# Optimization experiments

Hardware: AMD Instinct MI355X
Metric: run time of the kernel (lower is better)

Reference implementation:

```python
import jax, jax.numpy as jnp
import numpy as np

B, H, NQ, NK, D = 2, 16, 4096, 4096, 64


def _attn_with_lse(q, k, v, scale):
    # q: [B,H,p,d], k: [B,H,s,d], v: [B,H,s,dv]
    s = jnp.einsum('bhqd,bhkd->bhqk', q, k) * scale
    lse = jax.nn.logsumexp(s, axis=-1, keepdims=True)  # [B,H,p,1]
    p = jnp.exp(s - lse)
    o = jnp.einsum('bhqk,bhkd->bhqd', p, v)
    return o, lse


def setup_inputs() -> dict:
    key = jax.random.key(0)
    k1, k2, k3 = jax.random.split(key, 3)
    return {
        'query': jax.random.normal(k1, (B, H, NQ, D), dtype=jnp.float32),
        'key': jax.random.normal(k2, (B, H, NK, D), dtype=jnp.float32),
        'value': jax.random.normal(k3, (B, H, NK, D), dtype=jnp.float32),
        'n_query_groups': 4,
        'n_key_groups': 4,
    }


def reference(query, key, value, n_query_groups, n_key_groups):
    b, h, nq, d = query.shape
    nk = key.shape[2]
    m, n = int(n_query_groups), int(n_key_groups)
    scale = d ** (-0.5)
    pq, pk = nq // m, nk // n  # group sizes n_gp
    c0, c1 = m // 2, n // 2   # center groups c_gp

    # representative query/key blocks
    q_gp = query[:, :, c0 * pq:(c0 + 1) * pq, :]              # [B,H,pq,d]
    k_gp = key[:, :, c1 * pk:(c1 + 1) * pk, :]                # [B,H,pk,d]
    # value chunks concatenated on feature dim (zero-padding of q/k in the
    # original leaves the dot products unchanged, so we skip it)
    v_gp = value.reshape(b, h, n, pk, d).transpose(0, 1, 3, 2, 4).reshape(b, h, pk, n * d)
    attn_gp, lse_gp = _attn_with_lse(q_gp, k_gp, v_gp, scale)  # [B,H,pq,n*d], [B,H,pq,1]

    # sample one key per key group (torch uses random.randint; fixed to 0 here)
    k_picked = 0
    k_sample = key[:, :, k_picked::pk, :]                      # [B,H,n,d]
    w = jnp.einsum('bhqd,bhnd->bhqn', query, k_sample)         # [B,H,nq,n]
    w_gps = w.reshape(b, h, m, pq, n)
    norm_gps = jnp.linalg.norm(w_gps, axis=-2)                 # [B,H,m,n]
    s_gps = norm_gps / norm_gps[:, :, c0, c1][:, :, None, None]

    v_sum = value.reshape(b, h, n, pk, d).sum(axis=3)          # [B,H,n,d]
    om = jnp.maximum(1.0 - s_gps, 0.0)                         # clamp(1-s, min=0)
    num_part1 = om[:, :, :, :, None, None] * v_sum[:, :, None, :, None, :]  # [B,H,m,n,1,d]
    den_part1 = (om * pk)[:, :, :, :, None, None]              # [B,H,m,n,1,1]

    lse_exp = jnp.exp(lse_gp)                                  # [B,H,pq,1]
    unnorm = lse_exp * attn_gp                                 # [B,H,pq,n*d]
    attn_gps = unnorm.reshape(b, h, pq, n, d).transpose(0, 1, 3, 2, 4)  # [B,H,n,pq,d]
    num_part2 = s_gps[:, :, :, :, None, None] * attn_gps[:, :, None, :, :, :]  # [B,H,m,n,pq,d]
    den_part2 = s_gps[:, :, :, :, None, None] * lse_exp[:, :, None, None, :, :]  # [B,H,m,n,pq,1]

    num_agg = (num_part1 + num_part2).sum(axis=3)              # [B,H,m,pq,d]
    den_agg = (den_part1 + den_part2).sum(axis=3)              # [B,H,m,pq,1]

    attn = (num_agg / den_agg).reshape(b, h, nq, d)
    lse = jnp.log(den_agg).reshape(b, h, nq, 1)
    return attn, lse
```

## Files before the change

kernel.cpp:

```cpp
#include <hip/hip_runtime.h>
#include <hip/hip_bf16.h>


#define BH_TOT 32
#define SEQ    4096
#define DIM    64
#define PQ     1024

#define QB_OFF 34816u
#define KB_OFF (QB_OFF + 4u*1024u*1024u)
#define VB_OFF (KB_OFF + 4u*1024u*1024u)
#define WS_NEED (VB_OFF + 16u*1024u*1024u)

#define QSCALE 0.1803368801111204f

typedef __attribute__((ext_vector_type(8))) short bf16x8;
typedef __attribute__((ext_vector_type(4))) short bf16x4;
typedef __attribute__((ext_vector_type(4))) float f32x4;
typedef __attribute__((ext_vector_type(4))) _Float16 f16x4;
typedef __attribute__((ext_vector_type(8))) _Float16 f16x8;

__device__ __forceinline__ short f2bf(float x) {
    unsigned u = __float_as_uint(x);
    u = u + 0x7fffu + ((u >> 16) & 1u);
    return (short)(u >> 16);
}
__device__ __forceinline__ float bf2f(unsigned short h) {
    return __uint_as_float(((unsigned)h) << 16);
}

__global__ __launch_bounds__(256) void prep_norm2(
    const float* __restrict__ query, const float* __restrict__ key,
    float* __restrict__ ws)
{
    __shared__ float ksm[4][64];
    __shared__ float wsum[4][16];
    const int t = threadIdx.x;
    const int bh = blockIdx.x >> 2, gi = blockIdx.x & 3;
    if (t < 64) ws[512 + blockIdx.x * 64 + t] = 0.f;
    ksm[t >> 6][t & 63] = key[((size_t)bh * SEQ + (size_t)(t >> 6) * PQ) * DIM + (t & 63)];
    __syncthreads();
    const int wv = t >> 6, lane = t & 63, c = lane & 15, hi = lane >> 4;
    bf16x8 bb0, bb1;
#pragma unroll
    for (int j = 0; j < 8; ++j) {
        bb0[j] = (c < 4) ? f2bf(ksm[c][hi * 8 + j]) : (short)0;
        bb1[j] = (c < 4) ? f2bf(ksm[c][32 + hi * 8 + j]) : (short)0;
    }
    float acc0 = 0.f, acc1 = 0.f, acc2 = 0.f, acc3 = 0.f;
    const float* qbase = query + ((size_t)bh * SEQ + (size_t)gi * PQ) * DIM;
    for (int it = 0; it < 16; ++it) {
        const int row = (wv * 16 + it) * 16 + c;
        const float* qp = qbase + (size_t)row * 64 + hi * 8;
        float4 a0 = *(const float4*)qp;
        float4 a1 = *(const float4*)(qp + 4);
        float4 a2 = *(const float4*)(qp + 32);
        float4 a3 = *(const float4*)(qp + 36);
        bf16x8 qa0, qa1;
        qa0[0] = f2bf(a0.x); qa0[1] = f2bf(a0.y); qa0[2] = f2bf(a0.z); qa0[3] = f2bf(a0.w);
        qa0[4] = f2bf(a1.x); qa0[5] = f2bf(a1.y); qa0[6] = f2bf(a1.z); qa0[7] = f2bf(a1.w);
        qa1[0] = f2bf(a2.x); qa1[1] = f2bf(a2.y); qa1[2] = f2bf(a2.z); qa1[3] = f2bf(a2.w);
        qa1[4] = f2bf(a3.x); qa1[5] = f2bf(a3.y); qa1[6] = f2bf(a3.z); qa1[7] = f2bf(a3.w);
        f32x4 s = (f32x4){0.f, 0.f, 0.f, 0.f};
        s = __builtin_amdgcn_mfma_f32_16x16x32_bf16(qa0, bb0, s, 0, 0, 0);
        s = __builtin_amdgcn_mfma_f32_16x16x32_bf16(qa1, bb1, s, 0, 0, 0);
        acc0 += s[0] * s[0]; acc1 += s[1] * s[1];
        acc2 += s[2] * s[2]; acc3 += s[3] * s[3];
    }
    float asum = acc0 + acc1 + acc2 + acc3;
    asum += __shfl_xor(asum, 16);
    asum += __shfl_xor(asum, 32);
    if (lane < 16) wsum[wv][lane] = asum;
    __syncthreads();
    if (t < 4) ws[bh * 16 + gi * 4 + t] = wsum[0][t] + wsum[1][t] + wsum[2][t] + wsum[3][t];
}

__global__ __launch_bounds__(256) void conv_qk(
    const float* __restrict__ query, const float* __restrict__ key,
    char* __restrict__ wsb)
{
    const int t = threadIdx.x;
    if (blockIdx.x < 512) {
        const int bh = blockIdx.x >> 4, qt = blockIdx.x & 15;
#pragma unroll
        for (int i = 0; i < 2; ++i) {
            const int sid = t + i * 256;
            const int mt = sid >> 7, kh = (sid >> 6) & 1, lane = sid & 63;
            const int c = lane & 15, hi = lane >> 4;
            const float* p = query + ((size_t)bh * SEQ + 2048 + qt * 64 + mt * 16 + c) * DIM
                             + kh * 32 + hi * 8;
            float4 a = *(const float4*)p, b = *(const float4*)(p + 4);
            bf16x8 h;
            h[0] = f2bf(a.x * QSCALE); h[1] = f2bf(a.y * QSCALE);
            h[2] = f2bf(a.z * QSCALE); h[3] = f2bf(a.w * QSCALE);
            h[4] = f2bf(b.x * QSCALE); h[5] = f2bf(b.y * QSCALE);
            h[6] = f2bf(b.z * QSCALE); h[7] = f2bf(b.w * QSCALE);
            const size_t fidx = ((size_t)(bh * 16 + qt) * 4 + mt) * 2 + kh;
            *(bf16x8*)(wsb + QB_OFF + fidx * 1024 + lane * 16) = h;
        }
    } else {
        const int b2 = blockIdx.x - 512;
        const int bh = b2 >> 4, kc = b2 & 15;
#pragma unroll
        for (int i = 0; i < 2; ++i) {
            const int sid = t + i * 256;
            const int kh = sid >> 8, nt = (sid >> 6) & 3, lane = sid & 63;
            const int c = lane & 15, hi = lane >> 4;
            const float* p = key + ((size_t)bh * SEQ + 2048 + kc * 64 + nt * 16 + c) * DIM
                             + kh * 32 + hi * 8;
            float4 a = *(const float4*)p, b = *(const float4*)(p + 4);
            bf16x8 h;
            h[0] = f2bf(a.x); h[1] = f2bf(a.y); h[2] = f2bf(a.z); h[3] = f2bf(a.w);
            h[4] = f2bf(b.x); h[5] = f2bf(b.y); h[6] = f2bf(b.z); h[7] = f2bf(b.w);
            const size_t fidx = ((size_t)(bh * 16 + kc) * 2 + kh) * 4 + nt;
            *(bf16x8*)(wsb + KB_OFF + fidx * 1024 + lane * 16) = h;
        }
    }
}

__global__ __launch_bounds__(256) void conv_v(
    const float* __restrict__ value, char* __restrict__ wsb, float* __restrict__ ws)
{
    __shared__ float Ls[64][68];
    __shared__ float ps[4][64];
    const int t = threadIdx.x;
    const int blk = blockIdx.x;
    const int bh = blk >> 6, gj = (blk >> 4) & 3, kc = blk & 15;
    const float* src = value + ((size_t)bh * SEQ + gj * PQ + kc * 64) * DIM;
#pragma unroll
    for (int i = 0; i < 4; ++i) {
        const int u = t + i * 256;
        const int row = u >> 4, c4 = (u & 15) * 4;
        *(float4*)&Ls[row][c4] = *(const float4*)(src + row * 64 + c4);
    }
    __syncthreads();
    {
        const int d = t & 63, rg = t >> 6;
        float s = 0.f;
#pragma unroll
        for (int i = 0; i < 16; ++i) s += Ls[rg * 16 + i][d];
        ps[rg][d] = s;
    }
    __syncthreads();
    if (t < 64) {
        float tot = ps[0][t] + ps[1][t] + ps[2][t] + ps[3][t];
        atomicAdd(&ws[512 + bh * 256 + gj * 64 + t], tot);
    }
#pragma unroll
    for (int i = 0; i < 2; ++i) {
        const int sid = t + i * 256;
        const int pl = sid >> 8, dt = (sid >> 6) & 3, lane = sid & 63;
        const int c = lane & 15, hi = lane >> 4;
        f16x8 h;
#pragma unroll
        for (int j = 0; j < 8; ++j)
            h[j] = (_Float16)Ls[pl * 32 + hi * 8 + j][dt * 16 + c];
        const size_t off = ((((size_t)(bh * 4 + gj) * 32 + kc * 2 + pl) * 4 + dt) * 64 + lane) * 16;
        *(f16x8*)(wsb + VB_OFF + off) = h;
    }
}

__global__ __launch_bounds__(256, 4) void kattn4(
    const char* __restrict__ wsb, float* __restrict__ out)
{
    __shared__ union {
        _Float16 Pf[2][2][2][512];
        float Uf[32][257];
    } lds;
    __shared__ float Llds[32];

    const int blk = blockIdx.x;
    const int slot = blk >> 3;
    const int bh = (blk & 7) * 4 + (slot >> 5);
    const int qt = slot & 31;
    const int t = threadIdx.x;
    const int w = t >> 6, lane = t & 63;
    const int c = lane & 15, hi = lane >> 4;

    bf16x8 aq[2][2];
#pragma unroll
    for (int qt2 = 0; qt2 < 2; ++qt2) {
        const int s = qt * 2 + qt2;
        const size_t fr = ((size_t)(bh * 16 + (s >> 2)) * 4 + (s & 3)) * 2;
        aq[qt2][0] = *(const bf16x8*)(wsb + QB_OFF + fr * 1024 + lane * 16);
        aq[qt2][1] = *(const bf16x8*)(wsb + QB_OFF + (fr + 1) * 1024 + lane * 16);
    }
    const char* kb = wsb + KB_OFF + ((size_t)(bh * 16) * 8) * 1024 + (size_t)w * 1024 + lane * 16;
    const char* vb = wsb + VB_OFF + ((size_t)(bh * 4 + w) * 128) * 1024 + lane * 16;

    f32x4 Uacc[2][4];
#pragma unroll
    for (int mt = 0; mt < 2; ++mt)
#pragma unroll
        for (int dt = 0; dt < 4; ++dt)
            Uacc[mt][dt] = (f32x4){0.f, 0.f, 0.f, 0.f};
    f32x4 Lacc[2];
    Lacc[0] = (f32x4){0.f, 0.f, 0.f, 0.f};
    Lacc[1] = (f32x4){0.f, 0.f, 0.f, 0.f};
    f16x8 kOnes;
#pragma unroll
    for (int j = 0; j < 8; ++j) kOnes[j] = (_Float16)1.f;

    const int k0 = w * 16 + hi * 4;
    const int pspan = k0 >> 5;
    const int pidx = (c + 16 * ((k0 & 31) >> 3)) * 8 + (k0 & 7);

    bf16x8 bk0 = *(const bf16x8*)(kb);
    bf16x8 bk1 = *(const bf16x8*)(kb + 4096);

    for (int kc = 0; kc < 16; ++kc) {
        const int buf = kc & 1;
        const char* vcb = vb + (size_t)kc * 8192;
        f16x8 vf[8];
#pragma unroll
        for (int u = 0; u < 8; ++u) vf[u] = *(const f16x8*)(vcb + u * 1024);
        f32x4 sacc[2];
        __builtin_amdgcn_s_setprio(1);
#pragma unroll
        for (int qt2 = 0; qt2 < 2; ++qt2) {
            f32x4 s = (f32x4){0.f, 0.f, 0.f, 0.f};
            s = __builtin_amdgcn_mfma_f32_16x16x32_bf16(bk0, aq[qt2][0], s, 0, 0, 0);
            s = __builtin_amdgcn_mfma_f32_16x16x32_bf16(bk1, aq[qt2][1], s, 0, 0, 0);
            sacc[qt2] = s;
        }
        __builtin_amdgcn_s_setprio(0);
        if (kc < 15) {
            bk0 = *(const bf16x8*)(kb + (size_t)(kc + 1) * 8192);
            bk1 = *(const bf16x8*)(kb + (size_t)(kc + 1) * 8192 + 4096);
        }
#pragma unroll
        for (int qt2 = 0; qt2 < 2; ++qt2) {
            f16x4 ph;
#pragma unroll
            for (int r = 0; r < 4; ++r)
                ph[r] = (_Float16)__builtin_amdgcn_exp2f(sacc[qt2][r]);
            *(f16x4*)&lds.Pf[buf][qt2][pspan][pidx] = ph;
        }
        asm volatile("s_waitcnt lgkmcnt(0)" ::: "memory");
        __builtin_amdgcn_s_barrier();
        f16x8 ap[2][2];
#pragma unroll
        for (int mt = 0; mt < 2; ++mt)
#pragma unroll
            for (int sp = 0; sp < 2; ++sp)
                ap[mt][sp] = *(const f16x8*)&lds.Pf[buf][mt][sp][lane * 8];
        __builtin_amdgcn_s_setprio(1);
#pragma unroll
        for (int mt = 0; mt < 2; ++mt) {
#pragma unroll
            for (int sp = 0; sp < 2; ++sp) {
                Uacc[mt][0] = __builtin_amdgcn_mfma_f32_16x16x32_f16(ap[mt][sp], vf[sp * 4 + 0], Uacc[mt][0], 0, 0, 0);
                Uacc[mt][1] = __builtin_amdgcn_mfma_f32_16x16x32_f16(ap[mt][sp], vf[sp * 4 + 1], Uacc[mt][1], 0, 0, 0);
                Uacc[mt][2] = __builtin_amdgcn_mfma_f32_16x16x32_f16(ap[mt][sp], vf[sp * 4 + 2], Uacc[mt][2], 0, 0, 0);
                Uacc[mt][3] = __builtin_amdgcn_mfma_f32_16x16x32_f16(ap[mt][sp], vf[sp * 4 + 3], Uacc[mt][3], 0, 0, 0);
                Lacc[mt]    = __builtin_amdgcn_mfma_f32_16x16x32_f16(ap[mt][sp], kOnes, Lacc[mt], 0, 0, 0);
            }
        }
        __builtin_amdgcn_s_setprio(0);
    }

    __syncthreads();
#pragma unroll
    for (int mt = 0; mt < 2; ++mt)
#pragma unroll
        for (int dt = 0; dt < 4; ++dt)
#pragma unroll
            for (int r = 0; r < 4; ++r)
                lds.Uf[mt * 16 + hi * 4 + r][w * 64 + dt * 16 + c] = Uacc[mt][dt][r];
    if (w == 0 && c == 0) {
#pragma unroll
        for (int mt = 0; mt < 2; ++mt)
#pragma unroll
            for (int r = 0; r < 4; ++r)
                Llds[mt * 16 + hi * 4 + r] = Lacc[mt][r];
    }
    __syncthreads();

    const float* wsf = (const float*)wsb;
    const float* nsq = wsf + (size_t)bh * 16;
    const float* vsw = wsf + 512 + (size_t)bh * 256;
    const int dd = t & 63, rq = t >> 6;
    float sg[4][4], ssum[4], omp[4], ov[4];
    const float inv22 = 1.0f / nsq[10];
#pragma unroll
    for (int gi = 0; gi < 4; ++gi) {
        float ss = 0.f, os = 0.f, ovv = 0.f;
#pragma unroll
        for (int gj = 0; gj < 4; ++gj) {
            float sgv = sqrtf(nsq[gi * 4 + gj] * inv22);
            sg[gi][gj] = sgv;
            ss += sgv;
            float om = fmaxf(1.0f - sgv, 0.0f);
            os += om;
            ovv += om * vsw[gj * 64 + dd];
        }
        ssum[gi] = ss; omp[gi] = os * 1024.0f; ov[gi] = ovv;
    }
    const size_t base = (size_t)bh * SEQ * DIM;
    float* attn_out = out + base;
    float* lse_out = out + (size_t)BH_TOT * SEQ * DIM + (size_t)bh * SEQ;
    for (int k = 0; k < 8; ++k) {
        const int r = k * 4 + rq;
        const float u0 = lds.Uf[r][dd];
        const float u1 = lds.Uf[r][64 + dd];
        const float u2 = lds.Uf[r][128 + dd];
        const float u3 = lds.Uf[r][192 + dd];
        const float Lr = Llds[r];
        const int orow = qt * 32 + r;
#pragma unroll
        for (int gi = 0; gi < 4; ++gi) {
            float num = ov[gi] + sg[gi][0] * u0 + sg[gi][1] * u1 + sg[gi][2] * u2 + sg[gi][3] * u3;
            float den = omp[gi] + ssum[gi] * Lr;
            attn_out[(size_t)(gi * 1024 + orow) * 64 + dd] = num * __builtin_amdgcn_rcpf(den);
            if (dd == gi) lse_out[gi * 1024 + orow] = __logf(den);
        }
    }
}

__global__ __launch_bounds__(256) void prep_vsum(
    const float* __restrict__ value, float* __restrict__ ws)
{
    __shared__ float part[16][16][4];
    const int t = threadIdx.x;
    const int bh = blockIdx.x >> 2, gj = blockIdx.x & 3;
    const float4* vv = (const float4*)(value + ((size_t)bh * SEQ + (size_t)gj * PQ) * DIM);
    const int c4 = t & 15, rg = t >> 4;
    float a0 = 0.f, a1 = 0.f, a2 = 0.f, a3 = 0.f;
    for (int r = rg; r < 1024; r += 16) {
        float4 x = vv[r * 16 + c4];
        a0 += x.x; a1 += x.y; a2 += x.z; a3 += x.w;
    }
    part[rg][c4][0] = a0; part[rg][c4][1] = a1;
    part[rg][c4][2] = a2; part[rg][c4][3] = a3;
    __syncthreads();
    if (t < 64) {
        const int cc = t >> 2, comp = t & 3;
        float s = 0.f;
#pragma unroll
        for (int g = 0; g < 16; ++g) s += part[g][cc][comp];
        ws[512 + bh * 256 + gj * 64 + cc * 4 + comp] = s;
    }
}

__global__ __launch_bounds__(256, 2) void kattn_fallback(
    const float* __restrict__ query, const float* __restrict__ key,
    const float* __restrict__ value, const float* __restrict__ ws,
    float* __restrict__ out)
{
    __shared__ union {
        struct { short Q[64][72]; short K[64][72]; short P[64][72]; } s;
        unsigned short U[64][264];
    } lds;
    __shared__ float Llds[64];
    const int blk = blockIdx.x;
    const int bh = blk >> 4, qt = blk & 15;
    const int t = threadIdx.x;
    const int w = t >> 6, lane = t & 63;
    const int c = lane & 15, hi = lane >> 4;
    const size_t base = (size_t)bh * SEQ * DIM;
    {
        const float* qp = query + base + (size_t)(2048 + qt * 64) * DIM;
#pragma unroll
        for (int k2 = 0; k2 < 4; ++k2) {
            int u = t + k2 * 256;
            int row = u >> 4, ci = (u & 15) * 4;
            float4 qv = *(const float4*)(qp + row * 64 + ci);
            bf16x4 h;
            h[0] = f2bf(qv.x); h[1] = f2bf(qv.y); h[2] = f2bf(qv.z); h[3] = f2bf(qv.w);
            *(bf16x4*)&lds.s.Q[row][ci] = h;
        }
    }
    __syncthreads();
    bf16x8 aq0 = *(const bf16x8*)&lds.s.Q[w * 16 + c][hi * 8];
    bf16x8 aq1 = *(const bf16x8*)&lds.s.Q[w * 16 + c][32 + hi * 8];
    f32x4 Uacc[4][4];
#pragma unroll
    for (int mt = 0; mt < 4; ++mt)
#pragma unroll
        for (int nt = 0; nt < 4; ++nt)
            Uacc[mt][nt] = (f32x4){0.f, 0.f, 0.f, 0.f};
    float Lacc[4] = {0.f, 0.f, 0.f, 0.f};
    const float* kp = key + base + (size_t)2048 * DIM;
    const float* vgrp = value + base + (size_t)w * PQ * DIM;
    for (int kc = 0; kc < 16; ++kc) {
        {
            const float* kcp = kp + (size_t)kc * 64 * DIM;
#pragma unroll
            for (int k2 = 0; k2 < 4; ++k2) {
                int u = t + k2 * 256;
                int row = u >> 4, ci = (u & 15) * 4;
                float4 kv = *(const float4*)(kcp + row * 64 + ci);
                bf16x4 h;
                h[0] = f2bf(kv.x); h[1] = f2bf(kv.y); h[2] = f2bf(kv.z); h[3] = f2bf(kv.w);
                *(bf16x4*)&lds.s.K[row][ci] = h;
            }
        }
        __syncthreads();
        f32x4 sacc[4];
#pragma unroll
        for (int nt = 0; nt < 4; ++nt) sacc[nt] = (f32x4){0.f, 0.f, 0.f, 0.f};
#pragma unroll
        for (int nt = 0; nt < 4; ++nt) {
            bf16x8 bk = *(const bf16x8*)&lds.s.K[nt * 16 + c][hi * 8];
            sacc[nt] = __builtin_amdgcn_mfma_f32_16x16x32_bf16(aq0, bk, sacc[nt], 0, 0, 0);
        }
#pragma unroll
        for (int nt = 0; nt < 4; ++nt) {
            bf16x8 bk = *(const bf16x8*)&lds.s.K[nt * 16 + c][32 + hi * 8];
            sacc[nt] = __builtin_amdgcn_mfma_f32_16x16x32_bf16(aq1, bk, sacc[nt], 0, 0, 0);
        }
        float p[4][4];
#pragma unroll
        for (int nt = 0; nt < 4; ++nt)
#pragma unroll
            for (int r = 0; r < 4; ++r)
                p[nt][r] = __expf(sacc[nt][r] * 0.125f);
#pragma unroll
        for (int r = 0; r < 4; ++r) {
            float rs = p[0][r] + p[1][r] + p[2][r] + p[3][r];
            rs += __shfl_xor(rs, 1); rs += __shfl_xor(rs, 2);
            rs += __shfl_xor(rs, 4); rs += __shfl_xor(rs, 8);
            Lacc[r] += rs;
        }
#pragma unroll
        for (int nt = 0; nt < 4; ++nt)
#pragma unroll
            for (int r = 0; r < 4; ++r)
                lds.s.P[w * 16 + hi * 4 + r][nt * 16 + c] = (unsigned short)f2bf(p[nt][r]);
        __syncthreads();
        bf16x8 ap2[4][2];
#pragma unroll
        for (int mt = 0; mt < 4; ++mt) {
            ap2[mt][0] = *(const bf16x8*)&lds.s.P[mt * 16 + c][hi * 8];
            ap2[mt][1] = *(const bf16x8*)&lds.s.P[mt * 16 + c][32 + hi * 8];
        }
        const float* vp = vgrp + (size_t)kc * 64 * DIM;
#pragma unroll
        for (int kt = 0; kt < 2; ++kt) {
#pragma unroll
            for (int nt = 0; nt < 4; ++nt) {
                const float* vpp = vp + (kt * 32 + hi * 8) * 64 + nt * 16 + c;
                bf16x8 bv;
#pragma unroll
                for (int j = 0; j < 8; ++j) bv[j] = f2bf(vpp[j * 64]);
#pragma unroll
                for (int mt = 0; mt < 4; ++mt)
                    Uacc[mt][nt] = __builtin_amdgcn_mfma_f32_16x16x32_bf16(ap2[mt][kt], bv, Uacc[mt][nt], 0, 0, 0);
            }
        }
        __syncthreads();
    }
#pragma unroll
    for (int mt = 0; mt < 4; ++mt)
#pragma unroll
        for (int nt = 0; nt < 4; ++nt)
#pragma unroll
            for (int r = 0; r < 4; ++r)
                lds.U[mt * 16 + hi * 4 + r][w * 64 + nt * 16 + c] =
                    (unsigned short)f2bf(Uacc[mt][nt][r]);
    if (c == 0) {
#pragma unroll
        for (int r = 0; r < 4; ++r) Llds[w * 16 + hi * 4 + r] = Lacc[r];
    }
    __syncthreads();
    const float* nsq = ws + bh * 16;
    const float* vsw = ws + 512 + bh * 256;
    const int dd = t & 63, rq = t >> 6;
    float sg[4][4], ssum[4], omp[4], ov[4];
    const float inv22 = 1.0f / nsq[10];
#pragma unroll
    for (int gi = 0; gi < 4; ++gi) {
        float ss = 0.f, os = 0.f, ovv = 0.f;
#pragma unroll
        for (int gj = 0; gj < 4; ++gj) {
            float sgv = sqrtf(nsq[gi * 4 + gj] * inv22);
            sg[gi][gj] = sgv;
            ss += sgv;
            float om = fmaxf(1.0f - sgv, 0.0f);
            os += om;
            ovv += om * vsw[gj * 64 + dd];
        }
        ssum[gi] = ss; omp[gi] = os * 1024.0f; ov[gi] = ovv;
    }
    float* attn_out = out + base;
    float* lse_out = out + (size_t)BH_TOT * SEQ * DIM + (size_t)bh * SEQ;
    for (int k = 0; k < 16; ++k) {
        const int r = k * 4 + rq;
        const float u0 = bf2f(lds.U[r][dd]);
        const float u1 = bf2f(lds.U[r][64 + dd]);
        const float u2 = bf2f(lds.U[r][128 + dd]);
        const float u3 = bf2f(lds.U[r][192 + dd]);
        const float Lr = Llds[r];
        const int orow = qt * 64 + r;
#pragma unroll
        for (int gi = 0; gi < 4; ++gi) {
            float num = ov[gi] + sg[gi][0] * u0 + sg[gi][1] * u1 + sg[gi][2] * u2 + sg[gi][3] * u3;
            float den = omp[gi] + ssum[gi] * Lr;
            attn_out[(size_t)(gi * 1024 + orow) * 64 + dd] = num / den;
            if (dd == gi) lse_out[gi * 1024 + orow] = __logf(den);
        }
    }
}

extern "C" void kernel_launch(void* const* d_in, const int* in_sizes, int n_in,
                              void* d_out, int out_size, void* d_ws, size_t ws_size,
                              hipStream_t stream)
{
    (void)in_sizes; (void)n_in; (void)out_size;
    const float* query = (const float*)d_in[0];
    const float* key   = (const float*)d_in[1];
    const float* value = (const float*)d_in[2];
    float* ws   = (float*)d_ws;
    char*  wsb  = (char*)d_ws;
    float* outp = (float*)d_out;

    prep_norm2<<<128, 256, 0, stream>>>(query, key, ws);
    if (ws_size >= WS_NEED) {
        conv_qk<<<1024, 256, 0, stream>>>(query, key, wsb);
        conv_v<<<2048, 256, 0, stream>>>(value, wsb, ws);
        kattn4<<<1024, 256, 0, stream>>>(wsb, outp);
    } else {
        prep_vsum<<<128, 256, 0, stream>>>(value, ws);
        kattn_fallback<<<512, 256, 0, stream>>>(query, key, value, ws, outp);
    }
}
```

Measured before the change: 179.4 us.

## Fuse norm, value conversion and Q/K conversion prep kernels into one launch

```diff
diff --git a/kernel.cpp b/kernel.cpp
--- a/kernel.cpp
+++ b/kernel.cpp
@@ -27,6 +27,291 @@
 }
 __device__ __forceinline__ float bf2f(unsigned short h) {
     return __uint_as_float(((unsigned)h) << 16);
+}
+
+__global__ __launch_bounds__(256) void mega_prep(
+    const float* __restrict__ query, const float* __restrict__ key,
+    const float* __restrict__ value, float* __restrict__ ws,
+    char* __restrict__ wsb)
+{
+    __shared__ union {
+        struct { float ksm[4][64]; float wsum[4][16]; } n;
+        struct { float Ls[64][68]; float ps[4][64]; } v;
+    } sm;
+    const int t = threadIdx.x;
+    const int bid = blockIdx.x;
+
+    if (bid < 512) {
+        const int bh = bid >> 4, gi = (bid >> 2) & 3, chunk = bid & 3;
+        sm.n.ksm[t >> 6][t & 63] =
+            key[((size_t)bh * SEQ + (size_t)(t >> 6) * PQ) * DIM + (t & 63)];
+        __syncthreads();
+        const int wv = t >> 6, lane = t & 63, c = lane & 15, hi = lane >> 4;
+        bf16x8 bb0, bb1;
+#pragma unroll
+        for (int j = 0; j < 8; ++j) {
+            bb0[j] = (c < 4) ? f2bf(sm.n.ksm[c][hi * 8 + j]) : (short)0;
+            bb1[j] = (c < 4) ? f2bf(sm.n.ksm[c][32 + hi * 8 + j]) : (short)0;
+        }
+        float acc0 = 0.f, acc1 = 0.f, acc2 = 0.f, acc3 = 0.f;
+        const float* qbase = query +
+            ((size_t)bh * SEQ + (size_t)gi * PQ + (size_t)chunk * 256) * DIM;
+#pragma unroll
+        for (int it = 0; it < 4; ++it) {
+            const int row = (wv * 4 + it) * 16 + c;
+            const float* qp = qbase + (size_t)row * 64 + hi * 8;
+            float4 a0 = *(const float4*)qp;
+            float4 a1 = *(const float4*)(qp + 4);
+            float4 a2 = *(const float4*)(qp + 32);
+            float4 a3 = *(const float4*)(qp + 36);
+            bf16x8 qa0, qa1;
+            qa0[0] = f2bf(a0.x); qa0[1] = f2bf(a0.y); qa0[2] = f2bf(a0.z); qa0[3] = f2bf(a0.w);
+            qa0[4] = f2bf(a1.x); qa0[5] = f2bf(a1.y); qa0[6] = f2bf(a1.z); qa0[7] = f2bf(a1.w);
+            qa1[0] = f2bf(a2.x); qa1[1] = f2bf(a2.y); qa1[2] = f2bf(a2.z); qa1[3] = f2bf(a2.w);
+            qa1[4] = f2bf(a3.x); qa1[5] = f2bf(a3.y); qa1[6] = f2bf(a3.z); qa1[7] = f2bf(a3.w);
+            f32x4 s = (f32x4){0.f, 0.f, 0.f, 0.f};
+            s = __builtin_amdgcn_mfma_f32_16x16x32_bf16(qa0, bb0, s, 0, 0, 0);
+            s = __builtin_amdgcn_mfma_f32_16x16x32_bf16(qa1, bb1, s, 0, 0, 0);
+            acc0 += s[0] * s[0]; acc1 += s[1] * s[1];
+            acc2 += s[2] * s[2]; acc3 += s[3] * s[3];
+        }
+        float asum = acc0 + acc1 + acc2 + acc3;
+        asum += __shfl_xor(asum, 16);
+        asum += __shfl_xor(asum, 32);
+        if (lane < 16) sm.n.wsum[wv][lane] = asum;
+        __syncthreads();
+        if (t < 4)
+            atomicAdd(&ws[bh * 16 + gi * 4 + t],
+                      sm.n.wsum[0][t] + sm.n.wsum[1][t] + sm.n.wsum[2][t] + sm.n.wsum[3][t]);
+    } else if (bid < 2560) {
+        const int blk = bid - 512;
+        const int bh = blk >> 6, gj = (blk >> 4) & 3, kc = blk & 15;
+        const float* src = value + ((size_t)bh * SEQ + gj * PQ + kc * 64) * DIM;
+#pragma unroll
+        for (int i = 0; i < 4; ++i) {
+            const int u = t + i * 256;
+            const int row = u >> 4, c4 = (u & 15) * 4;
+            *(float4*)&sm.v.Ls[row][c4] = *(const float4*)(src + row * 64 + c4);
+        }
+        __syncthreads();
+        {
+            const int d = t & 63, rg = t >> 6;
+            float s = 0.f;
+#pragma unroll
+            for (int i = 0; i < 16; ++i) s += sm.v.Ls[rg * 16 + i][d];
+            sm.v.ps[rg][d] = s;
+        }
+        __syncthreads();
+        if (t < 64) {
+            float tot = sm.v.ps[0][t] + sm.v.ps[1][t] + sm.v.ps[2][t] + sm.v.ps[3][t];
+            atomicAdd(&ws[512 + bh * 256 + gj * 64 + t], tot);
+        }
+#pragma unroll
+        for (int i = 0; i < 2; ++i) {
+            const int sid = t + i * 256;
+            const int pl = sid >> 8, dt = (sid >> 6) & 3, lane = sid & 63;
+            const int c = lane & 15, hi = lane >> 4;
+            f16x8 h;
+#pragma unroll
+            for (int j = 0; j < 8; ++j)
+                h[j] = (_Float16)sm.v.Ls[pl * 32 + hi * 8 + j][dt * 16 + c];
+            const size_t off = ((((size_t)(bh * 4 + gj) * 32 + kc * 2 + pl) * 4 + dt) * 64 + lane) * 16;
+            *(f16x8*)(wsb + VB_OFF + off) = h;
+        }
+    } else if (bid < 3072) {
+        const int qb = bid - 2560;
+        const int bh = qb >> 4, qt = qb & 15;
+#pragma unroll
+        for (int i = 0; i < 2; ++i) {
+            const int sid = t + i * 256;
+            const int mt = sid >> 7, kh = (sid >> 6) & 1, lane = sid & 63;
+            const int c = lane & 15, hi = lane >> 4;
+            const float* p = query + ((size_t)bh * SEQ + 2048 + qt * 64 + mt * 16 + c) * DIM
+                             + kh * 32 + hi * 8;
+            float4 a = *(const float4*)p, b = *(const float4*)(p + 4);
+            bf16x8 h;
+            h[0] = f2bf(a.x * QSCALE); h[1] = f2bf(a.y * QSCALE);
+            h[2] = f2bf(a.z * QSCALE); h[3] = f2bf(a.w * QSCALE);
+            h[4] = f2bf(b.x * QSCALE); h[5] = f2bf(b.y * QSCALE);
+            h[6] = f2bf(b.z * QSCALE); h[7] = f2bf(b.w * QSCALE);
+            const size_t fidx = ((size_t)(bh * 16 + qt) * 4 + mt) * 2 + kh;
+            *(bf16x8*)(wsb + QB_OFF + fidx * 1024 + lane * 16) = h;
+        }
+    } else {
+        const int b2 = bid - 3072;
+        const int bh = b2 >> 4, kc = b2 & 15;
+#pragma unroll
+        for (int i = 0; i < 2; ++i) {
+            const int sid = t + i * 256;
+            const int kh = sid >> 8, nt = (sid >> 6) & 3, lane = sid & 63;
+            const int c = lane & 15, hi = lane >> 4;
+            const float* p = key + ((size_t)bh * SEQ + 2048 + kc * 64 + nt * 16 + c) * DIM
+                             + kh * 32 + hi * 8;
+            float4 a = *(const float4*)p, b = *(const float4*)(p + 4);
+            bf16x8 h;
+            h[0] = f2bf(a.x); h[1] = f2bf(a.y); h[2] = f2bf(a.z); h[3] = f2bf(a.w);
+            h[4] = f2bf(b.x); h[5] = f2bf(b.y); h[6] = f2bf(b.z); h[7] = f2bf(b.w);
+            const size_t fidx = ((size_t)(bh * 16 + kc) * 2 + kh) * 4 + nt;
+            *(bf16x8*)(wsb + KB_OFF + fidx * 1024 + lane * 16) = h;
+        }
+    }
+}
+
+__global__ __launch_bounds__(256, 4) void kattn4(
+    const char* __restrict__ wsb, float* __restrict__ out)
+{
+    __shared__ union {
+        _Float16 Pf[2][2][2][512];
+        float Uf[32][257];
+    } lds;
+    __shared__ float Llds[32];
+
+    const int blk = blockIdx.x;
+    const int slot = blk >> 3;
+    const int bh = (blk & 7) * 4 + (slot >> 5);
+    const int qt = slot & 31;
+    const int t = threadIdx.x;
+    const int w = t >> 6, lane = t & 63;
+    const int c = lane & 15, hi = lane >> 4;
+
+    bf16x8 aq[2][2];
+#pragma unroll
+    for (int qt2 = 0; qt2 < 2; ++qt2) {
+        const int s = qt * 2 + qt2;
+        const size_t fr = ((size_t)(bh * 16 + (s >> 2)) * 4 + (s & 3)) * 2;
+        aq[qt2][0] = *(const bf16x8*)(wsb + QB_OFF + fr * 1024 + lane * 16);
+        aq[qt2][1] = *(const bf16x8*)(wsb + QB_OFF + (fr + 1) * 1024 + lane * 16);
+    }
+    const char* kb = wsb + KB_OFF + ((size_t)(bh * 16) * 8) * 1024 + (size_t)w * 1024 + lane * 16;
+    const char* vb = wsb + VB_OFF + ((size_t)(bh * 4 + w) * 128) * 1024 + lane * 16;
+
+    f32x4 Uacc[2][4];
+#pragma unroll
+    for (int mt = 0; mt < 2; ++mt)
+#pragma unroll
+        for (int dt = 0; dt < 4; ++dt)
+            Uacc[mt][dt] = (f32x4){0.f, 0.f, 0.f, 0.f};
+    f32x4 Lacc[2];
+    Lacc[0] = (f32x4){0.f, 0.f, 0.f, 0.f};
+    Lacc[1] = (f32x4){0.f, 0.f, 0.f, 0.f};
+    f16x8 kOnes;
+#pragma unroll
+    for (int j = 0; j < 8; ++j) kOnes[j] = (_Float16)1.f;
+
+    const int k0 = w * 16 + hi * 4;
+    const int pspan = k0 >> 5;
+    const int pidx = (c + 16 * ((k0 & 31) >> 3)) * 8 + (k0 & 7);
+
+    bf16x8 bk0 = *(const bf16x8*)(kb);
+    bf16x8 bk1 = *(const bf16x8*)(kb + 4096);
+
+    for (int kc = 0; kc < 16; ++kc) {
+        const int buf = kc & 1;
+        const char* vcb = vb + (size_t)kc * 8192;
+        f16x8 vf[8];
+#pragma unroll
+        for (int u = 0; u < 8; ++u) vf[u] = *(const f16x8*)(vcb + u * 1024);
+        f32x4 sacc[2];
+        __builtin_amdgcn_s_setprio(1);
+#pragma unroll
+        for (int qt2 = 0; qt2 < 2; ++qt2) {
+            f32x4 s = (f32x4){0.f, 0.f, 0.f, 0.f};
+            s = __builtin_amdgcn_mfma_f32_16x16x32_bf16(bk0, aq[qt2][0], s, 0, 0, 0);
+            s = __builtin_amdgcn_mfma_f32_16x16x32_bf16(bk1, aq[qt2][1], s, 0, 0, 0);
+            sacc[qt2] = s;
+        }
+        __builtin_amdgcn_s_setprio(0);
+        if (kc < 15) {
+            bk0 = *(const bf16x8*)(kb + (size_t)(kc + 1) * 8192);
+            bk1 = *(const bf16x8*)(kb + (size_t)(kc + 1) * 8192 + 4096);
+        }
+#pragma unroll
+        for (int qt2 = 0; qt2 < 2; ++qt2) {
+            f16x4 ph;
+#pragma unroll
+            for (int r = 0; r < 4; ++r)
+                ph[r] = (_Float16)__builtin_amdgcn_exp2f(sacc[qt2][r]);
+            *(f16x4*)&lds.Pf[buf][qt2][pspan][pidx] = ph;
+        }
+        asm volatile("s_waitcnt lgkmcnt(0)" ::: "memory");
+        __builtin_amdgcn_s_barrier();
+        f16x8 ap[2][2];
+#pragma unroll
+        for (int mt = 0; mt < 2; ++mt)
+#pragma unroll
+            for (int sp = 0; sp < 2; ++sp)
+                ap[mt][sp] = *(const f16x8*)&lds.Pf[buf][mt][sp][lane * 8];
+        __builtin_amdgcn_s_setprio(1);
+#pragma unroll
+        for (int mt = 0; mt < 2; ++mt) {
+#pragma unroll
+            for (int sp = 0; sp < 2; ++sp) {
+                Uacc[mt][0] = __builtin_amdgcn_mfma_f32_16x16x32_f16(ap[mt][sp], vf[sp * 4 + 0], Uacc[mt][0], 0, 0, 0);
+                Uacc[mt][1] = __builtin_amdgcn_mfma_f32_16x16x32_f16(ap[mt][sp], vf[sp * 4 + 1], Uacc[mt][1], 0, 0, 0);
+                Uacc[mt][2] = __builtin_amdgcn_mfma_f32_16x16x32_f16(ap[mt][sp], vf[sp * 4 + 2], Uacc[mt][2], 0, 0, 0);
+                Uacc[mt][3] = __builtin_amdgcn_mfma_f32_16x16x32_f16(ap[mt][sp], vf[sp * 4 + 3], Uacc[mt][3], 0, 0, 0);
+                Lacc[mt]    = __builtin_amdgcn_mfma_f32_16x16x32_f16(ap[mt][sp], kOnes, Lacc[mt], 0, 0, 0);
+            }
+        }
+        __builtin_amdgcn_s_setprio(0);
+    }
+
+    __syncthreads();
+#pragma unroll
+    for (int mt = 0; mt < 2; ++mt)
+#pragma unroll
+        for (int dt = 0; dt < 4; ++dt)
+#pragma unroll
+            for (int r = 0; r < 4; ++r)
+                lds.Uf[mt * 16 + hi * 4 + r][w * 64 + dt * 16 + c] = Uacc[mt][dt][r];
+    if (w == 0 && c == 0) {
+#pragma unroll
+        for (int mt = 0; mt < 2; ++mt)
+#pragma unroll
+            for (int r = 0; r < 4; ++r)
+                Llds[mt * 16 + hi * 4 + r] = Lacc[mt][r];
+    }
+    __syncthreads();
+
+    const float* wsf = (const float*)wsb;
+    const float* nsq = wsf + (size_t)bh * 16;
+    const float* vsw = wsf + 512 + (size_t)bh * 256;
+    const int dd = t & 63, rq = t >> 6;
+    float sg[4][4], ssum[4], omp[4], ov[4];
+    const float inv22 = 1.0f / nsq[10];
+#pragma unroll
+    for (int gi = 0; gi < 4; ++gi) {
+        float ss = 0.f, os = 0.f, ovv = 0.f;
+#pragma unroll
+        for (int gj = 0; gj < 4; ++gj) {
+            float sgv = sqrtf(nsq[gi * 4 + gj] * inv22);
+            sg[gi][gj] = sgv;
+            ss += sgv;
+            float om = fmaxf(1.0f - sgv, 0.0f);
+            os += om;
+            ovv += om * vsw[gj * 64 + dd];
+        }
+        ssum[gi] = ss; omp[gi] = os * 1024.0f; ov[gi] = ovv;
+    }
+    const size_t base = (size_t)bh * SEQ * DIM;
+    float* attn_out = out + base;
+    float* lse_out = out + (size_t)BH_TOT * SEQ * DIM + (size_t)bh * SEQ;
+    for (int k = 0; k < 8; ++k) {
+        const int r = k * 4 + rq;
+        const float u0 = lds.Uf[r][dd];
+        const float u1 = lds.Uf[r][64 + dd];
+        const float u2 = lds.Uf[r][128 + dd];
+        const float u3 = lds.Uf[r][192 + dd];
+        const float Lr = Llds[r];
+        const int orow = qt * 32 + r;
+#pragma unroll
+        for (int gi = 0; gi < 4; ++gi) {
+            float num = ov[gi] + sg[gi][0] * u0 + sg[gi][1] * u1 + sg[gi][2] * u2 + sg[gi][3] * u3;
+            float den = omp[gi] + ssum[gi] * Lr;
+            attn_out[(size_t)(gi * 1024 + orow) * 64 + dd] = num * __builtin_amdgcn_rcpf(den);
+            if (dd == gi) lse_out[gi * 1024 + orow] = __logf(den);
+        }
+    }
 }
 
 __global__ __launch_bounds__(256) void prep_norm2(
@@ -75,248 +360,6 @@
     if (t < 4) ws[bh * 16 + gi * 4 + t] = wsum[0][t] + wsum[1][t] + wsum[2][t] + wsum[3][t];
 }
 
-__global__ __launch_bounds__(256) void conv_qk(
-    const float* __restrict__ query, const float* __restrict__ key,
-    char* __restrict__ wsb)
-{
-    const int t = threadIdx.x;
-    if (blockIdx.x < 512) {
-        const int bh = blockIdx.x >> 4, qt = blockIdx.x & 15;
-#pragma unroll
-        for (int i = 0; i < 2; ++i) {
-            const int sid = t + i * 256;
-            const int mt = sid >> 7, kh = (sid >> 6) & 1, lane = sid & 63;
-            const int c = lane & 15, hi = lane >> 4;
-            const float* p = query + ((size_t)bh * SEQ + 2048 + qt * 64 + mt * 16 + c) * DIM
-                             + kh * 32 + hi * 8;
-            float4 a = *(const float4*)p, b = *(const float4*)(p + 4);
-            bf16x8 h;
-            h[0] = f2bf(a.x * QSCALE); h[1] = f2bf(a.y * QSCALE);
-            h[2] = f2bf(a.z * QSCALE); h[3] = f2bf(a.w * QSCALE);
-            h[4] = f2bf(b.x * QSCALE); h[5] = f2bf(b.y * QSCALE);
-            h[6] = f2bf(b.z * QSCALE); h[7] = f2bf(b.w * QSCALE);
-            const size_t fidx = ((size_t)(bh * 16 + qt) * 4 + mt) * 2 + kh;
-            *(bf16x8*)(wsb + QB_OFF + fidx * 1024 + lane * 16) = h;
-        }
-    } else {
-        const int b2 = blockIdx.x - 512;
-        const int bh = b2 >> 4, kc = b2 & 15;
-#pragma unroll
-        for (int i = 0; i < 2; ++i) {
-            const int sid = t + i * 256;
-            const int kh = sid >> 8, nt = (sid >> 6) & 3, lane = sid & 63;
-            const int c = lane & 15, hi = lane >> 4;
-            const float* p = key + ((size_t)bh * SEQ + 2048 + kc * 64 + nt * 16 + c) * DIM
-                             + kh * 32 + hi * 8;
-            float4 a = *(const float4*)p, b = *(const float4*)(p + 4);
-            bf16x8 h;
-            h[0] = f2bf(a.x); h[1] = f2bf(a.y); h[2] = f2bf(a.z); h[3] = f2bf(a.w);
-            h[4] = f2bf(b.x); h[5] = f2bf(b.y); h[6] = f2bf(b.z); h[7] = f2bf(b.w);
-            const size_t fidx = ((size_t)(bh * 16 + kc) * 2 + kh) * 4 + nt;
-            *(bf16x8*)(wsb + KB_OFF + fidx * 1024 + lane * 16) = h;
-        }
-    }
-}
-
-__global__ __launch_bounds__(256) void conv_v(
-    const float* __restrict__ value, char* __restrict__ wsb, float* __restrict__ ws)
-{
-    __shared__ float Ls[64][68];
-    __shared__ float ps[4][64];
-    const int t = threadIdx.x;
-    const int blk = blockIdx.x;
-    const int bh = blk >> 6, gj = (blk >> 4) & 3, kc = blk & 15;
-    const float* src = value + ((size_t)bh * SEQ + gj * PQ + kc * 64) * DIM;
-#pragma unroll
-    for (int i = 0; i < 4; ++i) {
-        const int u = t + i * 256;
-        const int row = u >> 4, c4 = (u & 15) * 4;
-        *(float4*)&Ls[row][c4] = *(const float4*)(src + row * 64 + c4);
-    }
-    __syncthreads();
-    {
-        const int d = t & 63, rg = t >> 6;
-        float s = 0.f;
-#pragma unroll
-        for (int i = 0; i < 16; ++i) s += Ls[rg * 16 + i][d];
-        ps[rg][d] = s;
-    }
-    __syncthreads();
-    if (t < 64) {
-        float tot = ps[0][t] + ps[1][t] + ps[2][t] + ps[3][t];
-        atomicAdd(&ws[512 + bh * 256 + gj * 64 + t], tot);
-    }
-#pragma unroll
-    for (int i = 0; i < 2; ++i) {
-        const int sid = t + i * 256;
-        const int pl = sid >> 8, dt = (sid >> 6) & 3, lane = sid & 63;
-        const int c = lane & 15, hi = lane >> 4;
-        f16x8 h;
-#pragma unroll
-        for (int j = 0; j < 8; ++j)
-            h[j] = (_Float16)Ls[pl * 32 + hi * 8 + j][dt * 16 + c];
-        const size_t off = ((((size_t)(bh * 4 + gj) * 32 + kc * 2 + pl) * 4 + dt) * 64 + lane) * 16;
-        *(f16x8*)(wsb + VB_OFF + off) = h;
-    }
-}
-
-__global__ __launch_bounds__(256, 4) void kattn4(
-    const char* __restrict__ wsb, float* __restrict__ out)
-{
-    __shared__ union {
-        _Float16 Pf[2][2][2][512];
-        float Uf[32][257];
-    } lds;
-    __shared__ float Llds[32];
-
-    const int blk = blockIdx.x;
-    const int slot = blk >> 3;
-    const int bh = (blk & 7) * 4 + (slot >> 5);
-    const int qt = slot & 31;
-    const int t = threadIdx.x;
-    const int w = t >> 6, lane = t & 63;
-    const int c = lane & 15, hi = lane >> 4;
-
-    bf16x8 aq[2][2];
-#pragma unroll
-    for (int qt2 = 0; qt2 < 2; ++qt2) {
-        const int s = qt * 2 + qt2;
-        const size_t fr = ((size_t)(bh * 16 + (s >> 2)) * 4 + (s & 3)) * 2;
-        aq[qt2][0] = *(const bf16x8*)(wsb + QB_OFF + fr * 1024 + lane * 16);
-        aq[qt2][1] = *(const bf16x8*)(wsb + QB_OFF + (fr + 1) * 1024 + lane * 16);
-    }
-    const char* kb = wsb + KB_OFF + ((size_t)(bh * 16) * 8) * 1024 + (size_t)w * 1024 + lane * 16;
-    const char* vb = wsb + VB_OFF + ((size_t)(bh * 4 + w) * 128) * 1024 + lane * 16;
-
-    f32x4 Uacc[2][4];
-#pragma unroll
-    for (int mt = 0; mt < 2; ++mt)
-#pragma unroll
-        for (int dt = 0; dt < 4; ++dt)
-            Uacc[mt][dt] = (f32x4){0.f, 0.f, 0.f, 0.f};
-    f32x4 Lacc[2];
-    Lacc[0] = (f32x4){0.f, 0.f, 0.f, 0.f};
-    Lacc[1] = (f32x4){0.f, 0.f, 0.f, 0.f};
-    f16x8 kOnes;
-#pragma unroll
-    for (int j = 0; j < 8; ++j) kOnes[j] = (_Float16)1.f;
-
-    const int k0 = w * 16 + hi * 4;
-    const int pspan = k0 >> 5;
-    const int pidx = (c + 16 * ((k0 & 31) >> 3)) * 8 + (k0 & 7);
-
-    bf16x8 bk0 = *(const bf16x8*)(kb);
-    bf16x8 bk1 = *(const bf16x8*)(kb + 4096);
-
-    for (int kc = 0; kc < 16; ++kc) {
-        const int buf = kc & 1;
-        const char* vcb = vb + (size_t)kc * 8192;
-        f16x8 vf[8];
-#pragma unroll
-        for (int u = 0; u < 8; ++u) vf[u] = *(const f16x8*)(vcb + u * 1024);
-        f32x4 sacc[2];
-        __builtin_amdgcn_s_setprio(1);
-#pragma unroll
-        for (int qt2 = 0; qt2 < 2; ++qt2) {
-            f32x4 s = (f32x4){0.f, 0.f, 0.f, 0.f};
-            s = __builtin_amdgcn_mfma_f32_16x16x32_bf16(bk0, aq[qt2][0], s, 0, 0, 0);
-            s = __builtin_amdgcn_mfma_f32_16x16x32_bf16(bk1, aq[qt2][1], s, 0, 0, 0);
-            sacc[qt2] = s;
-        }
-        __builtin_amdgcn_s_setprio(0);
-        if (kc < 15) {
-            bk0 = *(const bf16x8*)(kb + (size_t)(kc + 1) * 8192);
-            bk1 = *(const bf16x8*)(kb + (size_t)(kc + 1) * 8192 + 4096);
-        }
-#pragma unroll
-        for (int qt2 = 0; qt2 < 2; ++qt2) {
-            f16x4 ph;
-#pragma unroll
-            for (int r = 0; r < 4; ++r)
-                ph[r] = (_Float16)__builtin_amdgcn_exp2f(sacc[qt2][r]);
-            *(f16x4*)&lds.Pf[buf][qt2][pspan][pidx] = ph;
-        }
-        asm volatile("s_waitcnt lgkmcnt(0)" ::: "memory");
-        __builtin_amdgcn_s_barrier();
-        f16x8 ap[2][2];
-#pragma unroll
-        for (int mt = 0; mt < 2; ++mt)
-#pragma unroll
-            for (int sp = 0; sp < 2; ++sp)
-                ap[mt][sp] = *(const f16x8*)&lds.Pf[buf][mt][sp][lane * 8];
-        __builtin_amdgcn_s_setprio(1);
-#pragma unroll
-        for (int mt = 0; mt < 2; ++mt) {
-#pragma unroll
-            for (int sp = 0; sp < 2; ++sp) {
-                Uacc[mt][0] = __builtin_amdgcn_mfma_f32_16x16x32_f16(ap[mt][sp], vf[sp * 4 + 0], Uacc[mt][0], 0, 0, 0);
-                Uacc[mt][1] = __builtin_amdgcn_mfma_f32_16x16x32_f16(ap[mt][sp], vf[sp * 4 + 1], Uacc[mt][1], 0, 0, 0);
-                Uacc[mt][2] = __builtin_amdgcn_mfma_f32_16x16x32_f16(ap[mt][sp], vf[sp * 4 + 2], Uacc[mt][2], 0, 0, 0);
-                Uacc[mt][3] = __builtin_amdgcn_mfma_f32_16x16x32_f16(ap[mt][sp], vf[sp * 4 + 3], Uacc[mt][3], 0, 0, 0);
-                Lacc[mt]    = __builtin_amdgcn_mfma_f32_16x16x32_f16(ap[mt][sp], kOnes, Lacc[mt], 0, 0, 0);
-            }
-        }
-        __builtin_amdgcn_s_setprio(0);
-    }
-
-    __syncthreads();
-#pragma unroll
-    for (int mt = 0; mt < 2; ++mt)
-#pragma unroll
-        for (int dt = 0; dt < 4; ++dt)
-#pragma unroll
-            for (int r = 0; r < 4; ++r)
-                lds.Uf[mt * 16 + hi * 4 + r][w * 64 + dt * 16 + c] = Uacc[mt][dt][r];
-    if (w == 0 && c == 0) {
-#pragma unroll
-        for (int mt = 0; mt < 2; ++mt)
-#pragma unroll
-            for (int r = 0; r < 4; ++r)
-                Llds[mt * 16 + hi * 4 + r] = Lacc[mt][r];
-    }
-    __syncthreads();
-
-    const float* wsf = (const float*)wsb;
-    const float* nsq = wsf + (size_t)bh * 16;
-    const float* vsw = wsf + 512 + (size_t)bh * 256;
-    const int dd = t & 63, rq = t >> 6;
-    float sg[4][4], ssum[4], omp[4], ov[4];
-    const float inv22 = 1.0f / nsq[10];
-#pragma unroll
-    for (int gi = 0; gi < 4; ++gi) {
-        float ss = 0.f, os = 0.f, ovv = 0.f;
-#pragma unroll
-        for (int gj = 0; gj < 4; ++gj) {
-            float sgv = sqrtf(nsq[gi * 4 + gj] * inv22);
-            sg[gi][gj] = sgv;
-            ss += sgv;
-            float om = fmaxf(1.0f - sgv, 0.0f);
-            os += om;
-            ovv += om * vsw[gj * 64 + dd];
-        }
-        ssum[gi] = ss; omp[gi] = os * 1024.0f; ov[gi] = ovv;
-    }
-    const size_t base = (size_t)bh * SEQ * DIM;
-    float* attn_out = out + base;
-    float* lse_out = out + (size_t)BH_TOT * SEQ * DIM + (size_t)bh * SEQ;
-    for (int k = 0; k < 8; ++k) {
-        const int r = k * 4 + rq;
-        const float u0 = lds.Uf[r][dd];
-        const float u1 = lds.Uf[r][64 + dd];
-        const float u2 = lds.Uf[r][128 + dd];
-        const float u3 = lds.Uf[r][192 + dd];
-        const float Lr = Llds[r];
-        const int orow = qt * 32 + r;
-#pragma unroll
-        for (int gi = 0; gi < 4; ++gi) {
-            float num = ov[gi] + sg[gi][0] * u0 + sg[gi][1] * u1 + sg[gi][2] * u2 + sg[gi][3] * u3;
-            float den = omp[gi] + ssum[gi] * Lr;
-            attn_out[(size_t)(gi * 1024 + orow) * 64 + dd] = num * __builtin_amdgcn_rcpf(den);
-            if (dd == gi) lse_out[gi * 1024 + orow] = __logf(den);
-        }
-    }
-}
-
 __global__ __launch_bounds__(256) void prep_vsum(
     const float* __restrict__ value, float* __restrict__ ws)
 {
@@ -514,12 +557,12 @@
     char*  wsb  = (char*)d_ws;
     float* outp = (float*)d_out;
 
-    prep_norm2<<<128, 256, 0, stream>>>(query, key, ws);
     if (ws_size >= WS_NEED) {
-        conv_qk<<<1024, 256, 0, stream>>>(query, key, wsb);
-        conv_v<<<2048, 256, 0, stream>>>(value, wsb, ws);
+        (void)hipMemsetAsync(d_ws, 0, QB_OFF, stream);
+        mega_prep<<<3584, 256, 0, stream>>>(query, key, value, ws, wsb);
         kattn4<<<1024, 256, 0, stream>>>(wsb, outp);
     } else {
+        prep_norm2<<<128, 256, 0, stream>>>(query, key, ws);
         prep_vsum<<<128, 256, 0, stream>>>(value, ws);
         kattn_fallback<<<512, 256, 0, stream>>>(query, key, value, ws, outp);
     }
```

After: 170.8 us. 1.05x faster.
